# Performance work log

Hardware: AMD Instinct MI355X
Metric: run time of the kernel (lower is better)

The kernel has to match this reference:

```python
import jax, jax.numpy as jnp
import numpy as np

SCALE = 0.08838834764831845  # 1/sqrt(128)
B, S, H, D = 16, 1, 16, 128
BLOCK_SIZE = 16
MAX_CTX = 1024
PROMPT_LEN = 512
NUM_BLOCKS = 2048
NEG_INF = -1e30


def setup_inputs() -> dict:
    key = jax.random.key(0)
    ks = jax.random.split(key, 8)
    hidden = H * D
    query = jax.random.normal(ks[0], (B, S, hidden), dtype=jnp.float32)
    k_new = jax.random.normal(ks[1], (B, S, hidden), dtype=jnp.float32)
    v_new = jax.random.normal(ks[2], (B, S, hidden), dtype=jnp.float32)
    key_cache = jax.random.normal(ks[3], (NUM_BLOCKS, H, BLOCK_SIZE, D), dtype=jnp.float32)
    value_cache = jax.random.normal(ks[4], (NUM_BLOCKS, H, D, BLOCK_SIZE), dtype=jnp.float32)
    # disjoint physical blocks per sequence: 32 prompt blocks + 64 decode blocks
    n_tbl = PROMPT_LEN // BLOCK_SIZE + MAX_CTX // BLOCK_SIZE  # 96
    block_tables = jnp.arange(B * n_tbl, dtype=jnp.int32).reshape(B, n_tbl)
    context_lens = jax.random.randint(ks[5], (B,), 1, MAX_CTX + 1, dtype=jnp.int32)
    # slot for the newly generated token (position context_lens-1 in decode region)
    pt_len = PROMPT_LEN // BLOCK_SIZE
    pos = context_lens - 1
    blk = block_tables[jnp.arange(B), pt_len + pos // BLOCK_SIZE]
    slot_mapping = (blk * BLOCK_SIZE + pos % BLOCK_SIZE).astype(jnp.int32).reshape(B, 1)
    attn_bias = jax.random.normal(ks[6], (B, H, 1, MAX_CTX), dtype=jnp.float32) * 0.1
    return {"query": query, "key": k_new, "value": v_new,
            "key_cache": key_cache, "value_cache": value_cache,
            "slot_mapping": slot_mapping, "block_tables": block_tables,
            "context_lens": context_lens, "attn_bias": attn_bias,
            "max_prompt_len": PROMPT_LEN}


def reference(query, key, value, key_cache, value_cache, slot_mapping,
              block_tables, context_lens, attn_bias, max_prompt_len):
    b, s, hidden = query.shape
    q = query.reshape(b * s, H, D)
    k_new = key.reshape(b * s, H, D)
    v_new = value.reshape(b * s, H, D)
    bs = value_cache.shape[3]
    # reshape_and_cache: write new K/V into paged caches at slot_mapping[:, -1]
    slots = slot_mapping[:, -1]
    bi, off = slots // bs, slots % bs
    key_cache = key_cache.at[bi, :, off, :].set(k_new)
    value_cache = value_cache.at[bi, :, :, off].set(v_new)
    # drop prompt blocks from the block table
    pt_len = (int(max_prompt_len) + bs - 1) // bs
    bt = block_tables[:, pt_len:]                      # [B, nb]
    nb = bt.shape[1]
    K = nb * bs
    keys = key_cache[bt]                               # [B, nb, H, bs, D]
    keys = keys.transpose(0, 2, 1, 3, 4).reshape(b, H, K, D)
    vals = value_cache[bt]                             # [B, nb, H, D, bs]
    vals = vals.transpose(0, 2, 1, 4, 3).reshape(b, H, K, D)
    scores = jnp.einsum('bhd,bhkd->bhk', q.reshape(b, H, D), keys) * SCALE
    scores = scores + attn_bias.astype(jnp.float32)[:, :, 0, :K]
    valid = jnp.arange(K, dtype=jnp.int32)[None, :] < context_lens[:, None]
    scores = jnp.where(valid[:, None, :], scores, NEG_INF)
    probs = jax.nn.softmax(scores, axis=-1)
    out = jnp.einsum('bhk,bhkd->bhd', probs, vals)
    return out.reshape(b, s, hidden)
```

## Files before the change

### kernel.cpp

```cpp
#include <hip/hip_runtime.h>
#include <cstdint>

#define NH 16
#define HD 128
#define BS 16
#define NTBL 96
#define PT_OFF 32
#define NSPLIT 16
#define SPLIT_BLOCKS 4
#define QK_SCALE 0.08838834764831845f
#define NEG_INF -1e30f
#define NB 16

__global__ __launch_bounds__(256) void attn_split_kernel(
    const float* __restrict__ q,
    const float* __restrict__ key_cache,
    const float* __restrict__ value_cache,
    const int* __restrict__ block_tables,
    const int* __restrict__ context_lens,
    const float* __restrict__ attn_bias,
    float* __restrict__ ws)
{
    const int s = blockIdx.x, h = blockIdx.y, b = blockIdx.z;
    const int ctx = context_lens[b];
    const int cap = ctx - 1;
    const int nbc = (ctx + 14) >> 4;
    const int jb0 = s * SPLIT_BLOCKS;
    if (jb0 >= nbc) return;
    const int nbl = min(SPLIT_BLOCKS, nbc - jb0);

    __shared__ float sc[64];
    __shared__ float sp[64];
    __shared__ int   sbt[SPLIT_BLOCKS];
    __shared__ float outA[128], outB[128];

    const int tid = threadIdx.x;
    const int wave = tid >> 6, lane = tid & 63;
    const int half = lane >> 5, lq = lane & 31;

    if (tid < SPLIT_BLOCKS) sbt[tid] = block_tables[b*NTBL + PT_OFF + jb0 + tid];

    const float4 qv = *(const float4*)(q + (size_t)b*2048 + h*HD + lq*4);
    __syncthreads();

    if (wave < nbl) {
        const int blk = sbt[wave];
        const float4* kb = (const float4*)(key_cache + ((size_t)blk*NH + h)*2048);
        #pragma unroll
        for (int i = 0; i < 8; ++i) {
            const float4 kv = kb[i*64 + lane];
            float part = kv.x*qv.x + kv.y*qv.y + kv.z*qv.z + kv.w*qv.w;
            part += __shfl_xor(part, 1);
            part += __shfl_xor(part, 2);
            part += __shfl_xor(part, 4);
            part += __shfl_xor(part, 8);
            part += __shfl_xor(part, 16);
            if (lq == 0) sc[wave*16 + i*2 + half] = part;
        }
    }
    __syncthreads();

    const int pos = lane;
    const int gpos = jb0*16 + pos;
    const bool valid = gpos < cap;
    const float x = valid
        ? (sc[pos]*QK_SCALE + attn_bias[((size_t)b*NH + h)*1024 + gpos])
        : NEG_INF;
    float m = x;
    #pragma unroll
    for (int msk = 32; msk >= 1; msk >>= 1) m = fmaxf(m, __shfl_xor(m, msk));
    const float pexp = valid ? __expf(x - m) : 0.0f;
    float l = pexp;
    #pragma unroll
    for (int msk = 32; msk >= 1; msk >>= 1) l += __shfl_xor(l, msk);
    if (wave == 0) sp[lane] = pexp;
    __syncthreads();

    const int team = tid >> 7, d = tid & 127;
    float acc = 0.0f;
    for (int jl = team; jl < nbl; jl += 2) {
        const int blk = sbt[jl];
        const float4* vb = (const float4*)(value_cache + ((size_t)blk*NH + h)*2048 + d*16);
        const float4 v0 = vb[0], v1 = vb[1], v2 = vb[2], v3 = vb[3];
        const float* pr = sp + jl*16;
        acc += pr[0]*v0.x + pr[1]*v0.y + pr[2]*v0.z  + pr[3]*v0.w;
        acc += pr[4]*v1.x + pr[5]*v1.y + pr[6]*v1.z  + pr[7]*v1.w;
        acc += pr[8]*v2.x + pr[9]*v2.y + pr[10]*v2.z + pr[11]*v2.w;
        acc += pr[12]*v3.x + pr[13]*v3.y + pr[14]*v3.z + pr[15]*v3.w;
    }
    if (team == 0) outA[d] = acc; else outB[d] = acc;
    __syncthreads();

    float* wsp = ws + (((size_t)b*NH + h)*NSPLIT + s)*130;
    if (tid < 128) wsp[tid] = outA[tid] + outB[tid];
    if (tid == 0) { wsp[128] = m; wsp[129] = l; }
}

__global__ __launch_bounds__(128) void reduce_kernel(
    const float* __restrict__ ws,
    const float* __restrict__ q,
    const float* __restrict__ k_new,
    const float* __restrict__ v_new,
    const int* __restrict__ context_lens,
    const float* __restrict__ attn_bias,
    float* __restrict__ out)
{
    const int h = blockIdx.x, b = blockIdx.y, d = threadIdx.x;
    const int wave = d >> 6, lane = d & 63;
    const int ctx = context_lens[b];
    const int cap = ctx - 1;
    const int nbc = (ctx + 14) >> 4;
    const int nsv = (nbc + SPLIT_BLOCKS - 1) >> 2;

    const size_t qoff = (size_t)b*2048 + h*HD + d;
    const float qd = q[qoff], kd = k_new[qoff], vd = v_new[qoff];

    float p = qd * kd;
    #pragma unroll
    for (int msk = 32; msk >= 1; msk >>= 1) p += __shfl_xor(p, msk);
    __shared__ float s2[2];
    if (lane == 0) s2[wave] = p;
    __syncthreads();
    const float score_new = (s2[0] + s2[1]) * QK_SCALE
                          + attn_bias[((size_t)b*NH + h)*1024 + cap];

    const float* base = ws + ((size_t)b*NH + h)*NSPLIT*130;
    float M = score_new;
    for (int s = 0; s < nsv; ++s) M = fmaxf(M, base[s*130 + 128]);
    const float w = __expf(score_new - M);
    float L = w, acc = w * vd;
    for (int s = 0; s < nsv; ++s) {
        const float e = __expf(base[s*130 + 128] - M);
        L   += base[s*130 + 129] * e;
        acc += base[s*130 + d] * e;
    }
    out[qoff] = acc / L;
}

extern "C" void kernel_launch(void* const* d_in, const int* in_sizes, int n_in,
                              void* d_out, int out_size, void* d_ws, size_t ws_size,
                              hipStream_t stream) {
    (void)in_sizes; (void)n_in; (void)out_size; (void)ws_size;
    const float* q        = (const float*)d_in[0];
    const float* k_new    = (const float*)d_in[1];
    const float* v_new    = (const float*)d_in[2];
    const float* kcache   = (const float*)d_in[3];
    const float* vcache   = (const float*)d_in[4];
    const int* btables    = (const int*)d_in[6];
    const int* ctx_lens   = (const int*)d_in[7];
    const float* bias     = (const float*)d_in[8];
    float* ws  = (float*)d_ws;
    float* out = (float*)d_out;

    attn_split_kernel<<<dim3(NSPLIT, NH, NB), 256, 0, stream>>>(
        q, kcache, vcache, btables, ctx_lens, bias, ws);
    reduce_kernel<<<dim3(NH, NB), 128, 0, stream>>>(
        ws, q, k_new, v_new, ctx_lens, bias, out);
}
```

Measured before the change: 451.6 us.

## Fuse split-K reduction into attention kernel via last-block atomic counter

Merges the separate reduce kernel into the split attention kernel. Each (b,h) group uses an atomic counter, and the last split to finish does the cross-split softmax combine together with the new-token contribution. It also issues the value-cache loads before the QK phase so they overlap with score computation. This removes one kernel launch and the dependency gap between kernels, but adds a memset launch and atomics/fences. It also raises register pressure from the prefetched value vectors.

```diff
diff --git a/kernel.cpp b/kernel.cpp
--- a/kernel.cpp
+++ b/kernel.cpp
@@ -3,7 +3,6 @@
 
 #define NH 16
 #define HD 128
-#define BS 16
 #define NTBL 96
 #define PT_OFF 32
 #define NSPLIT 16
@@ -12,36 +11,56 @@
 #define NEG_INF -1e30f
 #define NB 16
 
-__global__ __launch_bounds__(256) void attn_split_kernel(
+__global__ __launch_bounds__(256) void attn_fused_kernel(
     const float* __restrict__ q,
     const float* __restrict__ key_cache,
     const float* __restrict__ value_cache,
+    const float* __restrict__ k_new,
+    const float* __restrict__ v_new,
     const int* __restrict__ block_tables,
     const int* __restrict__ context_lens,
     const float* __restrict__ attn_bias,
-    float* __restrict__ ws)
+    float* __restrict__ ws,
+    unsigned* __restrict__ cnt,
+    float* __restrict__ out)
 {
     const int s = blockIdx.x, h = blockIdx.y, b = blockIdx.z;
     const int ctx = context_lens[b];
     const int cap = ctx - 1;
     const int nbc = (ctx + 14) >> 4;
+    const int nsv = (nbc + SPLIT_BLOCKS - 1) >> 2;
+    const int nact = (nsv > 0) ? nsv : 1;
+    if (s >= nact) return;
     const int jb0 = s * SPLIT_BLOCKS;
-    if (jb0 >= nbc) return;
     const int nbl = min(SPLIT_BLOCKS, nbc - jb0);
 
     __shared__ float sc[64];
     __shared__ float sp[64];
     __shared__ int   sbt[SPLIT_BLOCKS];
     __shared__ float outA[128], outB[128];
+    __shared__ float s2[2];
+    __shared__ int   lastFlag;
 
     const int tid = threadIdx.x;
     const int wave = tid >> 6, lane = tid & 63;
     const int half = lane >> 5, lq = lane & 31;
 
     if (tid < SPLIT_BLOCKS) sbt[tid] = block_tables[b*NTBL + PT_OFF + jb0 + tid];
-
     const float4 qv = *(const float4*)(q + (size_t)b*2048 + h*HD + lq*4);
     __syncthreads();
+
+    const int team = tid >> 7, d = tid & 127;
+    float4 va0, va1, va2, va3, vb0, vb1, vb2, vb3;
+    va0 = va1 = va2 = va3 = make_float4(0.f, 0.f, 0.f, 0.f);
+    vb0 = vb1 = vb2 = vb3 = make_float4(0.f, 0.f, 0.f, 0.f);
+    if (team < nbl) {
+        const float4* vp = (const float4*)(value_cache + ((size_t)sbt[team]*NH + h)*2048) + d*4;
+        va0 = vp[0]; va1 = vp[1]; va2 = vp[2]; va3 = vp[3];
+    }
+    if (team + 2 < nbl) {
+        const float4* vp = (const float4*)(value_cache + ((size_t)sbt[team+2]*NH + h)*2048) + d*4;
+        vb0 = vp[0]; vb1 = vp[1]; vb2 = vp[2]; vb3 = vp[3];
+    }
 
     if (wave < nbl) {
         const int blk = sbt[wave];
@@ -60,11 +79,10 @@
     }
     __syncthreads();
 
-    const int pos = lane;
-    const int gpos = jb0*16 + pos;
+    const int gpos = jb0*16 + lane;
     const bool valid = gpos < cap;
     const float x = valid
-        ? (sc[pos]*QK_SCALE + attn_bias[((size_t)b*NH + h)*1024 + gpos])
+        ? (sc[lane]*QK_SCALE + attn_bias[((size_t)b*NH + h)*1024 + gpos])
         : NEG_INF;
     float m = x;
     #pragma unroll
@@ -76,17 +94,20 @@
     if (wave == 0) sp[lane] = pexp;
     __syncthreads();
 
-    const int team = tid >> 7, d = tid & 127;
     float acc = 0.0f;
-    for (int jl = team; jl < nbl; jl += 2) {
-        const int blk = sbt[jl];
-        const float4* vb = (const float4*)(value_cache + ((size_t)blk*NH + h)*2048 + d*16);
-        const float4 v0 = vb[0], v1 = vb[1], v2 = vb[2], v3 = vb[3];
-        const float* pr = sp + jl*16;
-        acc += pr[0]*v0.x + pr[1]*v0.y + pr[2]*v0.z  + pr[3]*v0.w;
-        acc += pr[4]*v1.x + pr[5]*v1.y + pr[6]*v1.z  + pr[7]*v1.w;
-        acc += pr[8]*v2.x + pr[9]*v2.y + pr[10]*v2.z + pr[11]*v2.w;
-        acc += pr[12]*v3.x + pr[13]*v3.y + pr[14]*v3.z + pr[15]*v3.w;
+    {
+        const float* pr = sp + team*16;
+        acc += pr[0]*va0.x + pr[1]*va0.y + pr[2]*va0.z  + pr[3]*va0.w;
+        acc += pr[4]*va1.x + pr[5]*va1.y + pr[6]*va1.z  + pr[7]*va1.w;
+        acc += pr[8]*va2.x + pr[9]*va2.y + pr[10]*va2.z + pr[11]*va2.w;
+        acc += pr[12]*va3.x + pr[13]*va3.y + pr[14]*va3.z + pr[15]*va3.w;
+    }
+    {
+        const float* pr = sp + (team+2)*16;
+        acc += pr[0]*vb0.x + pr[1]*vb0.y + pr[2]*vb0.z  + pr[3]*vb0.w;
+        acc += pr[4]*vb1.x + pr[5]*vb1.y + pr[6]*vb1.z  + pr[7]*vb1.w;
+        acc += pr[8]*vb2.x + pr[9]*vb2.y + pr[10]*vb2.z + pr[11]*vb2.w;
+        acc += pr[12]*vb3.x + pr[13]*vb3.y + pr[14]*vb3.z + pr[15]*vb3.w;
     }
     if (team == 0) outA[d] = acc; else outB[d] = acc;
     __syncthreads();
@@ -94,47 +115,39 @@
     float* wsp = ws + (((size_t)b*NH + h)*NSPLIT + s)*130;
     if (tid < 128) wsp[tid] = outA[tid] + outB[tid];
     if (tid == 0) { wsp[128] = m; wsp[129] = l; }
-}
+    __syncthreads();
 
-__global__ __launch_bounds__(128) void reduce_kernel(
-    const float* __restrict__ ws,
-    const float* __restrict__ q,
-    const float* __restrict__ k_new,
-    const float* __restrict__ v_new,
-    const int* __restrict__ context_lens,
-    const float* __restrict__ attn_bias,
-    float* __restrict__ out)
-{
-    const int h = blockIdx.x, b = blockIdx.y, d = threadIdx.x;
-    const int wave = d >> 6, lane = d & 63;
-    const int ctx = context_lens[b];
-    const int cap = ctx - 1;
-    const int nbc = (ctx + 14) >> 4;
-    const int nsv = (nbc + SPLIT_BLOCKS - 1) >> 2;
-
-    const size_t qoff = (size_t)b*2048 + h*HD + d;
-    const float qd = q[qoff], kd = k_new[qoff], vd = v_new[qoff];
-
-    float p = qd * kd;
-    #pragma unroll
-    for (int msk = 32; msk >= 1; msk >>= 1) p += __shfl_xor(p, msk);
-    __shared__ float s2[2];
-    if (lane == 0) s2[wave] = p;
+    if (tid == 0) {
+        __threadfence();
+        unsigned old = __hip_atomic_fetch_add(cnt + b*NH + h, 1u,
+                                              __ATOMIC_ACQ_REL, __HIP_MEMORY_SCOPE_AGENT);
+        lastFlag = (old == (unsigned)(nact - 1)) ? 1 : 0;
+    }
     __syncthreads();
-    const float score_new = (s2[0] + s2[1]) * QK_SCALE
-                          + attn_bias[((size_t)b*NH + h)*1024 + cap];
-
-    const float* base = ws + ((size_t)b*NH + h)*NSPLIT*130;
-    float M = score_new;
-    for (int s = 0; s < nsv; ++s) M = fmaxf(M, base[s*130 + 128]);
-    const float w = __expf(score_new - M);
-    float L = w, acc = w * vd;
-    for (int s = 0; s < nsv; ++s) {
-        const float e = __expf(base[s*130 + 128] - M);
-        L   += base[s*130 + 129] * e;
-        acc += base[s*130 + d] * e;
+    if (lastFlag) {
+        __threadfence();
+        const size_t qoff = (size_t)b*2048 + h*HD + d;
+        float p = (tid < 128) ? q[qoff] * k_new[qoff] : 0.0f;
+        #pragma unroll
+        for (int msk = 32; msk >= 1; msk >>= 1) p += __shfl_xor(p, msk);
+        if (lane == 0 && wave < 2) s2[wave] = p;
+        __syncthreads();
+        if (tid < 128) {
+            const float score_new = (s2[0] + s2[1]) * QK_SCALE
+                                  + attn_bias[((size_t)b*NH + h)*1024 + cap];
+            const float* base = ws + ((size_t)b*NH + h)*NSPLIT*130;
+            float M = score_new;
+            for (int ss = 0; ss < nact; ++ss) M = fmaxf(M, base[ss*130 + 128]);
+            const float w = __expf(score_new - M);
+            float L = w, acc2 = w * v_new[qoff];
+            for (int ss = 0; ss < nact; ++ss) {
+                const float e = __expf(base[ss*130 + 128] - M);
+                L    += base[ss*130 + 129] * e;
+                acc2 += base[ss*130 + d] * e;
+            }
+            out[qoff] = acc2 / L;
+        }
     }
-    out[qoff] = acc / L;
 }
 
 extern "C" void kernel_launch(void* const* d_in, const int* in_sizes, int n_in,
@@ -150,10 +163,10 @@
     const int* ctx_lens   = (const int*)d_in[7];
     const float* bias     = (const float*)d_in[8];
     float* ws  = (float*)d_ws;
+    unsigned* cnt = (unsigned*)(ws + (size_t)NB*NH*NSPLIT*130);
     float* out = (float*)d_out;
 
-    attn_split_kernel<<<dim3(NSPLIT, NH, NB), 256, 0, stream>>>(
-        q, kcache, vcache, btables, ctx_lens, bias, ws);
-    reduce_kernel<<<dim3(NH, NB), 128, 0, stream>>>(
-        ws, q, k_new, v_new, ctx_lens, bias, out);
+    hipMemsetAsync(cnt, 0, NB*NH*sizeof(unsigned), stream);
+    attn_fused_kernel<<<dim3(NSPLIT, NH, NB), 256, 0, stream>>>(
+        q, kcache, vcache, k_new, v_new, btables, ctx_lens, bias, ws, cnt, out);
 }
```

Result: slower. 832.3 us (+84.3%).
